# Performance work log

Measured on AMD Instinct MI355X. Metric: run time of the kernel, lower is better.

## Reference

```python
import jax, jax.numpy as jnp
import numpy as np

B, S, D = 4, 1024, 1024      # batch, seq_len, hidden_size
I = 4096                     # intermediate_size
E = 8                        # num_experts
K = 2                        # top-k


def setup_inputs() -> dict:
    key = jax.random.key(0)
    ks = jax.random.split(key, 8)
    x = jax.random.normal(ks[0], (B, S, D), dtype=jnp.float32)
    gate_w = jax.random.normal(ks[1], (E, D), dtype=jnp.float32) * 0.02
    gate_b = jnp.zeros((E,), dtype=jnp.float32)
    w1 = jax.random.normal(ks[2], (E, I, D), dtype=jnp.float32) * 0.02
    b1 = jnp.zeros((E, I), dtype=jnp.float32)
    w2 = jax.random.normal(ks[3], (E, D, I), dtype=jnp.float32) * 0.02
    b2 = jnp.zeros((E, D), dtype=jnp.float32)
    return {"x": x, "gate_w": gate_w, "gate_b": gate_b,
            "w1": w1, "b1": b1, "w2": w2, "b2": b2}


def reference(x, gate_w, gate_b, w1, b1, w2, b2):
    b, s, d = x.shape
    xf = x.reshape(-1, d)                                  # [N, D]
    logits = xf @ gate_w.T + gate_b                        # [N, E]
    top_vals, top_idx = jax.lax.top_k(logits, K)           # [N, K]
    top_w = jax.nn.softmax(top_vals, axis=-1)              # softmax over the k selected logits

    # combine[n, e] = routing weight of token n for expert e (0 if not selected)
    n_tok = xf.shape[0]
    combine = jnp.zeros((n_tok, w1.shape[0]), dtype=x.dtype)
    combine = combine.at[jnp.arange(n_tok)[:, None], top_idx].add(top_w)

    out = jnp.zeros_like(xf)
    for e in range(w1.shape[0]):                           # small fixed loop over experts
        h = jax.nn.gelu(xf @ w1[e].T + b1[e], approximate=False)  # exact GELU (torch default)
        out = out + combine[:, e:e + 1] * (h @ w2[e].T + b2[e])
    return out.reshape(b, s, d)
```

## Files before the change

kernel.cpp:

```cpp
#include <hip/hip_runtime.h>
#include <math.h>

#define NTOK 4096
#define DDIM 1024
#define IDIM 4096
#define NEXP 8
#define MAXPAD 9216

typedef _Float16 f16x8 __attribute__((ext_vector_type(8)));
typedef _Float16 f16x4 __attribute__((ext_vector_type(4)));
typedef float    f32x4 __attribute__((ext_vector_type(4)));

__device__ __forceinline__ void glds16(const _Float16* g, _Float16* l) {
    __builtin_amdgcn_global_load_lds(
        (const __attribute__((address_space(1))) _Float16*)g,
        (__attribute__((address_space(3))) _Float16*)l, 16, 0, 0);
}

__device__ __forceinline__ float fast_gelu(float v) {
    float u = v * (0.7978845608f + 0.0356774081f * v * v);
    float ex = __builtin_amdgcn_exp2f(u * 2.8853900817779268f);
    float th = 1.0f - 2.0f * __builtin_amdgcn_rcpf(ex + 1.0f);
    return 0.5f * v * (1.0f + th);
}

__global__ void cvt_kernel(const float* __restrict__ src, _Float16* __restrict__ dst, int n4) {
    int i = blockIdx.x * blockDim.x + threadIdx.x;
    if (i >= n4) return;
    float4 v = ((const float4*)src)[i];
    f16x4 o = { (_Float16)v.x, (_Float16)v.y, (_Float16)v.z, (_Float16)v.w };
    ((f16x4*)dst)[i] = o;
}

__global__ void gate_kernel(const float* __restrict__ x, const float* __restrict__ gw,
                            const float* __restrict__ gb,
                            int* __restrict__ cnt, int* __restrict__ tok,
                            float* __restrict__ wgt) {
    int wave = threadIdx.x >> 6;
    int lane = threadIdx.x & 63;
    int token = blockIdx.x * 4 + wave;
    const float* xr = x + (size_t)token * DDIM;
    float xv[16];
#pragma unroll
    for (int j = 0; j < 16; ++j) xv[j] = xr[lane + 64 * j];
    float lg[NEXP];
#pragma unroll
    for (int e = 0; e < NEXP; ++e) {
        const float* g = gw + e * DDIM;
        float s = 0.f;
#pragma unroll
        for (int j = 0; j < 16; ++j) s += xv[j] * g[lane + 64 * j];
#pragma unroll
        for (int o = 32; o > 0; o >>= 1) s += __shfl_xor(s, o, 64);
        lg[e] = s + gb[e];
    }
    if (lane == 0) {
        int i0 = 0; float v0 = lg[0];
        for (int e = 1; e < NEXP; ++e) if (lg[e] > v0) { v0 = lg[e]; i0 = e; }
        int i1 = -1; float v1 = -3.0e38f;
        for (int e = 0; e < NEXP; ++e) { if (e == i0) continue; if (lg[e] > v1) { v1 = lg[e]; i1 = e; } }
        float e1 = expf(v1 - v0);
        float den = 1.f + e1;
        float w0 = 1.f / den;
        float w1 = e1 / den;
        int p0 = atomicAdd(&cnt[i0], 1);
        tok[i0 * NTOK + p0] = token; wgt[i0 * NTOK + p0] = w0;
        int p1 = atomicAdd(&cnt[i1], 1);
        tok[i1 * NTOK + p1] = token; wgt[i1 * NTOK + p1] = w1;
    }
}

__global__ void scan_kernel(const int* __restrict__ cnt, int* __restrict__ off) {
    if (threadIdx.x == 0) {
        int acc = 0;
        for (int e = 0; e < NEXP; ++e) { off[e] = acc; acc += ((cnt[e] + 127) >> 7) << 7; }
        off[NEXP] = acc;
    }
}

__global__ void gather_kernel(const float* __restrict__ x, const int* __restrict__ cnt,
                              const int* __restrict__ off, const int* __restrict__ tok,
                              _Float16* __restrict__ xg) {
    int row = blockIdx.x;
    if (row >= off[NEXP]) return;
    int e = 0;
    while (e < NEXP - 1 && row >= off[e + 1]) ++e;
    int r = row - off[e];
    int t = threadIdx.x;
    _Float16* dst = xg + (size_t)row * DDIM;
    if (r < cnt[e]) {
        int token = tok[e * NTOK + r];
        float4 v = ((const float4*)(x + (size_t)token * DDIM))[t];
        f16x4 o = { (_Float16)v.x, (_Float16)v.y, (_Float16)v.z, (_Float16)v.w };
        ((f16x4*)dst)[t] = o;
    } else {
        f16x4 z = {};
        ((f16x4*)dst)[t] = z;
    }
}

#define SBAR() do { __builtin_amdgcn_s_barrier(); asm volatile("" ::: "memory"); } while (0)
#define STA(b, s, ko) glds16(ap[s] + (ko), &As[b][((s) * 64 + wv * 8) * 64])
#define STB(b, s, ko) glds16(bp[s] + (ko), &Bs[b][((s) * 64 + wv * 8) * 64])
#define ARD(buf, row, kb) (*(const f16x8*)&As[buf][(row) * 64 + ((((kb) + fq) ^ ((row) & 7)) << 3)])
#define BRD(buf, row, kb) (*(const f16x8*)&Bs[buf][(row) * 64 + ((((kb) + fq) ^ ((row) & 7)) << 3)])

template <int KDIM, int NDIM, int NT, int EPI, int SPLIT>
__global__ __launch_bounds__(512, 2) void gemm256_kernel(
    const _Float16* __restrict__ A,
    const _Float16* __restrict__ Bw,
    const float* __restrict__ bias,
    const int* __restrict__ cnt, const int* __restrict__ off,
    const int* __restrict__ tok, const float* __restrict__ wgt,
    _Float16* __restrict__ Hout, float* __restrict__ Out) {
    const int e  = blockIdx.z / SPLIT;
    const int kc = blockIdx.z % SPLIT;
    constexpr int KB = KDIM / SPLIT;
    constexpr int NK = KB / 64;
    const int nt = (int)blockIdx.x % NT;
    const int mt = (int)blockIdx.x / NT;
    const int ce = cnt[e];
    if (mt >= ((ce + 255) >> 8)) return;
    const int rowbase = off[e] + mt * 256;
    const int colbase = nt * 256;

    __shared__ __align__(16) _Float16 As[2][256 * 64];
    __shared__ __align__(16) _Float16 Bs[2][256 * 64];

    const int tid = threadIdx.x;
    const int wv = tid >> 6, lane = tid & 63;
    const int wm = (wv >> 2) * 128;
    const int wn = (wv & 3) * 64;
    const int fr = lane & 15, fq = lane >> 4;

    const int srow = lane >> 3;
    const int scol = ((lane & 7) ^ srow) << 3;
    const _Float16* ap[4];
    const _Float16* bp[4];
#pragma unroll
    for (int s = 0; s < 4; ++s) {
        int ra = rowbase + s * 64 + wv * 8 + srow;
        if (ra > MAXPAD - 1) ra = MAXPAD - 1;
        ap[s] = A + (size_t)ra * KDIM + kc * KB + scol;
        bp[s] = Bw + ((size_t)e * NDIM + colbase + s * 64 + wv * 8 + srow) * KDIM + kc * KB + scol;
    }

    f32x4 acc[8][4] = {};

    STA(0, 0, 0); STA(0, 1, 0); STA(0, 2, 0); STA(0, 3, 0);
    STB(0, 0, 0); STB(0, 1, 0); STB(0, 2, 0); STB(0, 3, 0);

    for (int kt = 0; kt < NK; ++kt) {
        const int cur = kt & 1, nxt = cur ^ 1;
        const int ko = (kt + 1) * 64;
        f16x8 a[4], b[4];
        if (kt + 1 < NK) {
            STA(nxt, 0, ko); STA(nxt, 1, ko); STA(nxt, 2, ko); STA(nxt, 3, ko);
            STB(nxt, 0, ko); STB(nxt, 1, ko); STB(nxt, 2, ko); STB(nxt, 3, ko);
            asm volatile("s_waitcnt vmcnt(8)" ::: "memory");
        } else {
            asm volatile("s_waitcnt vmcnt(0)" ::: "memory");
        }
        SBAR();
#pragma unroll
        for (int i = 0; i < 4; ++i) a[i] = ARD(cur, wm + i * 16 + fr, 0);
#pragma unroll
        for (int j = 0; j < 4; ++j) b[j] = BRD(cur, wn + j * 16 + fr, 0);
        __builtin_amdgcn_s_setprio(1);
#pragma unroll
        for (int i = 0; i < 4; ++i)
#pragma unroll
            for (int j = 0; j < 4; ++j)
                acc[i][j] = __builtin_amdgcn_mfma_f32_16x16x32_f16(a[i], b[j], acc[i][j], 0, 0, 0);
        __builtin_amdgcn_s_setprio(0);
#pragma unroll
        for (int i = 0; i < 4; ++i) a[i] = ARD(cur, wm + 64 + i * 16 + fr, 0);
        __builtin_amdgcn_s_setprio(1);
#pragma unroll
        for (int i = 0; i < 4; ++i)
#pragma unroll
            for (int j = 0; j < 4; ++j)
                acc[i + 4][j] = __builtin_amdgcn_mfma_f32_16x16x32_f16(a[i], b[j], acc[i + 4][j], 0, 0, 0);
        __builtin_amdgcn_s_setprio(0);
#pragma unroll
        for (int i = 0; i < 4; ++i) a[i] = ARD(cur, wm + 64 + i * 16 + fr, 4);
#pragma unroll
        for (int j = 0; j < 4; ++j) b[j] = BRD(cur, wn + j * 16 + fr, 4);
        __builtin_amdgcn_s_setprio(1);
#pragma unroll
        for (int i = 0; i < 4; ++i)
#pragma unroll
            for (int j = 0; j < 4; ++j)
                acc[i + 4][j] = __builtin_amdgcn_mfma_f32_16x16x32_f16(a[i], b[j], acc[i + 4][j], 0, 0, 0);
        __builtin_amdgcn_s_setprio(0);
#pragma unroll
        for (int i = 0; i < 4; ++i) a[i] = ARD(cur, wm + i * 16 + fr, 4);
        __builtin_amdgcn_s_setprio(1);
#pragma unroll
        for (int i = 0; i < 4; ++i)
#pragma unroll
            for (int j = 0; j < 4; ++j)
                acc[i][j] = __builtin_amdgcn_mfma_f32_16x16x32_f16(a[i], b[j], acc[i][j], 0, 0, 0);
        __builtin_amdgcn_s_setprio(0);
        asm volatile("s_waitcnt lgkmcnt(0)" ::: "memory");
        SBAR();
    }

    const int rq = fq << 2;
    if constexpr (EPI == 1) {
        const int elim = off[e + 1];
#pragma unroll
        for (int q = 0; q < 8; ++q) {
            const int rbase = wm + ((q >> 2) * 64) + ((q & 3) * 16) + rq;
#pragma unroll
            for (int r = 0; r < 4; ++r) {
                const int grow = rowbase + rbase + r;
                if (grow < elim) {
#pragma unroll
                    for (int j = 0; j < 4; ++j) {
                        const int col = colbase + wn + j * 16 + fr;
                        float v = fast_gelu(acc[q][j][r] + bias[e * NDIM + col]);
                        Hout[(size_t)grow * NDIM + col] = (_Float16)v;
                    }
                }
            }
        }
    } else {
#pragma unroll
        for (int q = 0; q < 8; ++q) {
            const int rbase = wm + ((q >> 2) * 64) + ((q & 3) * 16) + rq;
#pragma unroll
            for (int r = 0; r < 4; ++r) {
                const int slot = mt * 256 + rbase + r;
                if (slot < ce) {
                    const int token = tok[e * NTOK + slot];
                    const float w = wgt[e * NTOK + slot];
#pragma unroll
                    for (int j = 0; j < 4; ++j) {
                        const int col = colbase + wn + j * 16 + fr;
                        float v = acc[q][j][r];
                        if (kc == 0) v += bias[e * NDIM + col];
                        unsafeAtomicAdd(&Out[(size_t)token * NDIM + col], w * v);
                    }
                }
            }
        }
    }
}

extern "C" void kernel_launch(void* const* d_in, const int* in_sizes, int n_in,
                              void* d_out, int out_size, void* d_ws, size_t ws_size,
                              hipStream_t stream) {
    const float* x      = (const float*)d_in[0];
    const float* gate_w = (const float*)d_in[1];
    const float* gate_b = (const float*)d_in[2];
    const float* w1     = (const float*)d_in[3];
    const float* b1     = (const float*)d_in[4];
    const float* w2     = (const float*)d_in[5];
    const float* b2     = (const float*)d_in[6];
    float* out = (float*)d_out;

    char* p = (char*)d_ws;
    _Float16* w1h  = (_Float16*)p; p += (size_t)NEXP * IDIM * DDIM * 2;
    _Float16* w2h  = (_Float16*)p; p += (size_t)NEXP * DDIM * IDIM * 2;
    _Float16* xg   = (_Float16*)p; p += (size_t)MAXPAD * DDIM * 2;
    _Float16* hbuf = (_Float16*)p; p += (size_t)MAXPAD * IDIM * 2;
    int*      tok  = (int*)p;      p += (size_t)NEXP * NTOK * 4;
    float*    wgt  = (float*)p;    p += (size_t)NEXP * NTOK * 4;
    int*      cnt  = (int*)p;      p += 128;
    int*      off  = (int*)p;      p += 128;

    hipMemsetAsync(cnt, 0, 128, stream);
    hipMemsetAsync(out, 0, (size_t)NTOK * DDIM * 4, stream);

    cvt_kernel<<<32768, 256, 0, stream>>>(w1, w1h, NEXP * IDIM * DDIM / 4);
    cvt_kernel<<<32768, 256, 0, stream>>>(w2, w2h, NEXP * DDIM * IDIM / 4);
    gate_kernel<<<NTOK / 4, 256, 0, stream>>>(x, gate_w, gate_b, cnt, tok, wgt);
    scan_kernel<<<1, 64, 0, stream>>>(cnt, off);
    gather_kernel<<<MAXPAD, 256, 0, stream>>>(x, cnt, off, tok, xg);

    gemm256_kernel<DDIM, IDIM, IDIM / 256, 1, 1>
        <<<dim3(16 * (IDIM / 256), 1, NEXP), 512, 0, stream>>>(
            xg, w1h, b1, cnt, off, tok, wgt, hbuf, (float*)nullptr);
    gemm256_kernel<IDIM, DDIM, DDIM / 256, 2, 2>
        <<<dim3(16 * (DDIM / 256), 1, NEXP * 2), 512, 0, stream>>>(
            hbuf, w2h, b2, cnt, off, tok, wgt, (_Float16*)nullptr, out);
}
```

Measured before the change: 784.8 us.

## Use persistent GEMM blocks over a device-built tile work queue, split-K to four

The scan kernel now builds compact work lists of (expert, m-tile, n-tile, k-chunk) items for both expert GEMMs. Each GEMM launches 256 persistent blocks that walk their list, replacing a large grid in which most blocks exited early. The second GEMM raises split-K from 2 to 4, giving more tiles to spread across CUs for load balance. The cost is twice as many float atomic adds into the output, plus an extra barrier per work item.

Result: slower. 842.2 us (+7.3%).

```diff
diff --git a/kernel.cpp b/kernel.cpp
--- a/kernel.cpp
+++ b/kernel.cpp
@@ -70,11 +70,24 @@
     }
 }
 
-__global__ void scan_kernel(const int* __restrict__ cnt, int* __restrict__ off) {
+__global__ void scan_kernel(const int* __restrict__ cnt, int* __restrict__ off,
+                            int* __restrict__ q1, int* __restrict__ q2) {
     if (threadIdx.x == 0) {
         int acc = 0;
         for (int e = 0; e < NEXP; ++e) { off[e] = acc; acc += ((cnt[e] + 127) >> 7) << 7; }
         off[NEXP] = acc;
+        int n1 = 0, n2 = 0;
+        for (int e = 0; e < NEXP; ++e) {
+            int mtiles = (cnt[e] + 255) >> 8;
+            for (int mt = 0; mt < mtiles; ++mt) {
+                for (int nt = 0; nt < IDIM / 256; ++nt)
+                    q1[n1++] = e | (mt << 4) | (nt << 12);
+                for (int kc = 0; kc < 4; ++kc)
+                    for (int nt = 0; nt < DDIM / 256; ++nt)
+                        q2[n2++] = e | (mt << 4) | (nt << 12) | (kc << 20);
+            }
+        }
+        off[10] = n1; off[11] = n2;
     }
 }
 
@@ -105,24 +118,17 @@
 #define ARD(buf, row, kb) (*(const f16x8*)&As[buf][(row) * 64 + ((((kb) + fq) ^ ((row) & 7)) << 3)])
 #define BRD(buf, row, kb) (*(const f16x8*)&Bs[buf][(row) * 64 + ((((kb) + fq) ^ ((row) & 7)) << 3)])
 
-template <int KDIM, int NDIM, int NT, int EPI, int SPLIT>
+template <int KDIM, int NDIM, int EPI, int SPLIT>
 __global__ __launch_bounds__(512, 2) void gemm256_kernel(
     const _Float16* __restrict__ A,
     const _Float16* __restrict__ Bw,
     const float* __restrict__ bias,
     const int* __restrict__ cnt, const int* __restrict__ off,
     const int* __restrict__ tok, const float* __restrict__ wgt,
-    _Float16* __restrict__ Hout, float* __restrict__ Out) {
-    const int e  = blockIdx.z / SPLIT;
-    const int kc = blockIdx.z % SPLIT;
+    _Float16* __restrict__ Hout, float* __restrict__ Out,
+    const int* __restrict__ qarr, const int* __restrict__ qn) {
     constexpr int KB = KDIM / SPLIT;
     constexpr int NK = KB / 64;
-    const int nt = (int)blockIdx.x % NT;
-    const int mt = (int)blockIdx.x / NT;
-    const int ce = cnt[e];
-    if (mt >= ((ce + 255) >> 8)) return;
-    const int rowbase = off[e] + mt * 256;
-    const int colbase = nt * 256;
 
     __shared__ __align__(16) _Float16 As[2][256 * 64];
     __shared__ __align__(16) _Float16 Bs[2][256 * 64];
@@ -132,115 +138,128 @@
     const int wm = (wv >> 2) * 128;
     const int wn = (wv & 3) * 64;
     const int fr = lane & 15, fq = lane >> 4;
-
     const int srow = lane >> 3;
     const int scol = ((lane & 7) ^ srow) << 3;
-    const _Float16* ap[4];
-    const _Float16* bp[4];
-#pragma unroll
-    for (int s = 0; s < 4; ++s) {
-        int ra = rowbase + s * 64 + wv * 8 + srow;
-        if (ra > MAXPAD - 1) ra = MAXPAD - 1;
-        ap[s] = A + (size_t)ra * KDIM + kc * KB + scol;
-        bp[s] = Bw + ((size_t)e * NDIM + colbase + s * 64 + wv * 8 + srow) * KDIM + kc * KB + scol;
-    }
-
-    f32x4 acc[8][4] = {};
-
-    STA(0, 0, 0); STA(0, 1, 0); STA(0, 2, 0); STA(0, 3, 0);
-    STB(0, 0, 0); STB(0, 1, 0); STB(0, 2, 0); STB(0, 3, 0);
-
-    for (int kt = 0; kt < NK; ++kt) {
-        const int cur = kt & 1, nxt = cur ^ 1;
-        const int ko = (kt + 1) * 64;
-        f16x8 a[4], b[4];
-        if (kt + 1 < NK) {
-            STA(nxt, 0, ko); STA(nxt, 1, ko); STA(nxt, 2, ko); STA(nxt, 3, ko);
-            STB(nxt, 0, ko); STB(nxt, 1, ko); STB(nxt, 2, ko); STB(nxt, 3, ko);
-            asm volatile("s_waitcnt vmcnt(8)" ::: "memory");
-        } else {
-            asm volatile("s_waitcnt vmcnt(0)" ::: "memory");
+    const int nwork = *qn;
+
+    for (int wi = blockIdx.x; wi < nwork; wi += gridDim.x) {
+        __syncthreads();
+        const int w = qarr[wi];
+        const int e  = w & 15;
+        const int mt = (w >> 4) & 63;
+        const int nt = (w >> 12) & 63;
+        const int kc = (w >> 20) & 7;
+        const int ce = cnt[e];
+        const int rowbase = off[e] + mt * 256;
+        const int colbase = nt * 256;
+
+        const _Float16* ap[4];
+        const _Float16* bp[4];
+#pragma unroll
+        for (int s = 0; s < 4; ++s) {
+            int ra = rowbase + s * 64 + wv * 8 + srow;
+            if (ra > MAXPAD - 1) ra = MAXPAD - 1;
+            ap[s] = A + (size_t)ra * KDIM + kc * KB + scol;
+            bp[s] = Bw + ((size_t)e * NDIM + colbase + s * 64 + wv * 8 + srow) * KDIM + kc * KB + scol;
         }
-        SBAR();
-#pragma unroll
-        for (int i = 0; i < 4; ++i) a[i] = ARD(cur, wm + i * 16 + fr, 0);
-#pragma unroll
-        for (int j = 0; j < 4; ++j) b[j] = BRD(cur, wn + j * 16 + fr, 0);
-        __builtin_amdgcn_s_setprio(1);
-#pragma unroll
-        for (int i = 0; i < 4; ++i)
-#pragma unroll
-            for (int j = 0; j < 4; ++j)
-                acc[i][j] = __builtin_amdgcn_mfma_f32_16x16x32_f16(a[i], b[j], acc[i][j], 0, 0, 0);
-        __builtin_amdgcn_s_setprio(0);
-#pragma unroll
-        for (int i = 0; i < 4; ++i) a[i] = ARD(cur, wm + 64 + i * 16 + fr, 0);
-        __builtin_amdgcn_s_setprio(1);
-#pragma unroll
-        for (int i = 0; i < 4; ++i)
-#pragma unroll
-            for (int j = 0; j < 4; ++j)
-                acc[i + 4][j] = __builtin_amdgcn_mfma_f32_16x16x32_f16(a[i], b[j], acc[i + 4][j], 0, 0, 0);
-        __builtin_amdgcn_s_setprio(0);
-#pragma unroll
-        for (int i = 0; i < 4; ++i) a[i] = ARD(cur, wm + 64 + i * 16 + fr, 4);
-#pragma unroll
-        for (int j = 0; j < 4; ++j) b[j] = BRD(cur, wn + j * 16 + fr, 4);
-        __builtin_amdgcn_s_setprio(1);
-#pragma unroll
-        for (int i = 0; i < 4; ++i)
-#pragma unroll
-            for (int j = 0; j < 4; ++j)
-                acc[i + 4][j] = __builtin_amdgcn_mfma_f32_16x16x32_f16(a[i], b[j], acc[i + 4][j], 0, 0, 0);
-        __builtin_amdgcn_s_setprio(0);
-#pragma unroll
-        for (int i = 0; i < 4; ++i) a[i] = ARD(cur, wm + i * 16 + fr, 4);
-        __builtin_amdgcn_s_setprio(1);
-#pragma unroll
-        for (int i = 0; i < 4; ++i)
-#pragma unroll
-            for (int j = 0; j < 4; ++j)
-                acc[i][j] = __builtin_amdgcn_mfma_f32_16x16x32_f16(a[i], b[j], acc[i][j], 0, 0, 0);
-        __builtin_amdgcn_s_setprio(0);
-        asm volatile("s_waitcnt lgkmcnt(0)" ::: "memory");
-        SBAR();
-    }
-
-    const int rq = fq << 2;
-    if constexpr (EPI == 1) {
-        const int elim = off[e + 1];
-#pragma unroll
-        for (int q = 0; q < 8; ++q) {
-            const int rbase = wm + ((q >> 2) * 64) + ((q & 3) * 16) + rq;
-#pragma unroll
-            for (int r = 0; r < 4; ++r) {
-                const int grow = rowbase + rbase + r;
-                if (grow < elim) {
-#pragma unroll
-                    for (int j = 0; j < 4; ++j) {
-                        const int col = colbase + wn + j * 16 + fr;
-                        float v = fast_gelu(acc[q][j][r] + bias[e * NDIM + col]);
-                        Hout[(size_t)grow * NDIM + col] = (_Float16)v;
+
+        f32x4 acc[8][4] = {};
+
+        STA(0, 0, 0); STA(0, 1, 0); STA(0, 2, 0); STA(0, 3, 0);
+        STB(0, 0, 0); STB(0, 1, 0); STB(0, 2, 0); STB(0, 3, 0);
+
+        for (int kt = 0; kt < NK; ++kt) {
+            const int cur = kt & 1, nxt = cur ^ 1;
+            const int ko = (kt + 1) * 64;
+            f16x8 a[4], b[4];
+            if (kt + 1 < NK) {
+                STA(nxt, 0, ko); STA(nxt, 1, ko); STA(nxt, 2, ko); STA(nxt, 3, ko);
+                STB(nxt, 0, ko); STB(nxt, 1, ko); STB(nxt, 2, ko); STB(nxt, 3, ko);
+                asm volatile("s_waitcnt vmcnt(8)" ::: "memory");
+            } else {
+                asm volatile("s_waitcnt vmcnt(0)" ::: "memory");
+            }
+            SBAR();
+#pragma unroll
+            for (int i = 0; i < 4; ++i) a[i] = ARD(cur, wm + i * 16 + fr, 0);
+#pragma unroll
+            for (int j = 0; j < 4; ++j) b[j] = BRD(cur, wn + j * 16 + fr, 0);
+            __builtin_amdgcn_s_setprio(1);
+#pragma unroll
+            for (int i = 0; i < 4; ++i)
+#pragma unroll
+                for (int j = 0; j < 4; ++j)
+                    acc[i][j] = __builtin_amdgcn_mfma_f32_16x16x32_f16(a[i], b[j], acc[i][j], 0, 0, 0);
+            __builtin_amdgcn_s_setprio(0);
+#pragma unroll
+            for (int i = 0; i < 4; ++i) a[i] = ARD(cur, wm + 64 + i * 16 + fr, 0);
+            __builtin_amdgcn_s_setprio(1);
+#pragma unroll
+            for (int i = 0; i < 4; ++i)
+#pragma unroll
+                for (int j = 0; j < 4; ++j)
+                    acc[i + 4][j] = __builtin_amdgcn_mfma_f32_16x16x32_f16(a[i], b[j], acc[i + 4][j], 0, 0, 0);
+            __builtin_amdgcn_s_setprio(0);
+#pragma unroll
+            for (int i = 0; i < 4; ++i) a[i] = ARD(cur, wm + 64 + i * 16 + fr, 4);
+#pragma unroll
+            for (int j = 0; j < 4; ++j) b[j] = BRD(cur, wn + j * 16 + fr, 4);
+            __builtin_amdgcn_s_setprio(1);
+#pragma unroll
+            for (int i = 0; i < 4; ++i)
+#pragma unroll
+                for (int j = 0; j < 4; ++j)
+                    acc[i + 4][j] = __builtin_amdgcn_mfma_f32_16x16x32_f16(a[i], b[j], acc[i + 4][j], 0, 0, 0);
+            __builtin_amdgcn_s_setprio(0);
+#pragma unroll
+            for (int i = 0; i < 4; ++i) a[i] = ARD(cur, wm + i * 16 + fr, 4);
+            __builtin_amdgcn_s_setprio(1);
+#pragma unroll
+            for (int i = 0; i < 4; ++i)
+#pragma unroll
+                for (int j = 0; j < 4; ++j)
+                    acc[i][j] = __builtin_amdgcn_mfma_f32_16x16x32_f16(a[i], b[j], acc[i][j], 0, 0, 0);
+            __builtin_amdgcn_s_setprio(0);
+            asm volatile("s_waitcnt lgkmcnt(0)" ::: "memory");
+            SBAR();
+        }
+
+        const int rq = fq << 2;
+        if constexpr (EPI == 1) {
+            const int elim = off[e + 1];
+#pragma unroll
+            for (int q = 0; q < 8; ++q) {
+                const int rbase = wm + ((q >> 2) * 64) + ((q & 3) * 16) + rq;
+#pragma unroll
+                for (int r = 0; r < 4; ++r) {
+                    const int grow = rowbase + rbase + r;
+                    if (grow < elim) {
+#pragma unroll
+                        for (int j = 0; j < 4; ++j) {
+                            const int col = colbase + wn + j * 16 + fr;
+                            float v = fast_gelu(acc[q][j][r] + bias[e * NDIM + col]);
+                            Hout[(size_t)grow * NDIM + col] = (_Float16)v;
+                        }
                     }
                 }
             }
-        }
-    } else {
-#pragma unroll
-        for (int q = 0; q < 8; ++q) {
-            const int rbase = wm + ((q >> 2) * 64) + ((q & 3) * 16) + rq;
-#pragma unroll
-            for (int r = 0; r < 4; ++r) {
-                const int slot = mt * 256 + rbase + r;
-                if (slot < ce) {
-                    const int token = tok[e * NTOK + slot];
-                    const float w = wgt[e * NTOK + slot];
-#pragma unroll
-                    for (int j = 0; j < 4; ++j) {
-                        const int col = colbase + wn + j * 16 + fr;
-                        float v = acc[q][j][r];
-                        if (kc == 0) v += bias[e * NDIM + col];
-                        unsafeAtomicAdd(&Out[(size_t)token * NDIM + col], w * v);
+        } else {
+#pragma unroll
+            for (int q = 0; q < 8; ++q) {
+                const int rbase = wm + ((q >> 2) * 64) + ((q & 3) * 16) + rq;
+#pragma unroll
+                for (int r = 0; r < 4; ++r) {
+                    const int slot = mt * 256 + rbase + r;
+                    if (slot < ce) {
+                        const int token = tok[e * NTOK + slot];
+                        const float ww = wgt[e * NTOK + slot];
+#pragma unroll
+                        for (int j = 0; j < 4; ++j) {
+                            const int col = colbase + wn + j * 16 + fr;
+                            float v = acc[q][j][r];
+                            if (kc == 0) v += bias[e * NDIM + col];
+                            unsafeAtomicAdd(&Out[(size_t)token * NDIM + col], ww * v);
+                        }
                     }
                 }
             }
@@ -269,6 +288,8 @@
     float*    wgt  = (float*)p;    p += (size_t)NEXP * NTOK * 4;
     int*      cnt  = (int*)p;      p += 128;
     int*      off  = (int*)p;      p += 128;
+    int*      q1   = (int*)p;      p += 4096;
+    int*      q2   = (int*)p;      p += 4096;
 
     hipMemsetAsync(cnt, 0, 128, stream);
     hipMemsetAsync(out, 0, (size_t)NTOK * DDIM * 4, stream);
@@ -276,13 +297,11 @@
     cvt_kernel<<<32768, 256, 0, stream>>>(w1, w1h, NEXP * IDIM * DDIM / 4);
     cvt_kernel<<<32768, 256, 0, stream>>>(w2, w2h, NEXP * DDIM * IDIM / 4);
     gate_kernel<<<NTOK / 4, 256, 0, stream>>>(x, gate_w, gate_b, cnt, tok, wgt);
-    scan_kernel<<<1, 64, 0, stream>>>(cnt, off);
+    scan_kernel<<<1, 64, 0, stream>>>(cnt, off, q1, q2);
     gather_kernel<<<MAXPAD, 256, 0, stream>>>(x, cnt, off, tok, xg);
 
-    gemm256_kernel<DDIM, IDIM, IDIM / 256, 1, 1>
-        <<<dim3(16 * (IDIM / 256), 1, NEXP), 512, 0, stream>>>(
-            xg, w1h, b1, cnt, off, tok, wgt, hbuf, (float*)nullptr);
-    gemm256_kernel<IDIM, DDIM, DDIM / 256, 2, 2>
-        <<<dim3(16 * (DDIM / 256), 1, NEXP * 2), 512, 0, stream>>>(
-            hbuf, w2h, b2, cnt, off, tok, wgt, (_Float16*)nullptr, out);
-}
+    gemm256_kernel<DDIM, IDIM, 1, 1><<<dim3(256), 512, 0, stream>>>(
+        xg, w1h, b1, cnt, off, tok, wgt, hbuf, (float*)nullptr, q1, off + 10);
+    gemm256_kernel<IDIM, DDIM, 2, 4><<<dim3(256), 512, 0, stream>>>(
+        hbuf, w2h, b2, cnt, off, tok, wgt, (_Float16*)nullptr, out, q2, off + 11);
+}
```
